# Kernel tuning notes

Hardware: AMD Instinct MI355X
Metric: run time of the kernel (lower is better)

The kernel has to match this reference:

```python
import jax, jax.numpy as jnp
import numpy as np

IGNORE_INDEX = -100
MTP_CE_FACTOR = 0.0
MTP_KL_FACTOR = 1.0

B, S, D, V = 2, 2048, 2048, 32000


def setup_inputs() -> dict:
    key = jax.random.key(0)
    k1, k2, k3, k4 = jax.random.split(key, 4)
    outputs = jax.random.normal(k1, (B, S, D), dtype=jnp.float32)
    mtp_outputs = jax.random.normal(k2, (B, S, D), dtype=jnp.float32)
    # LM-head weight (linear_projection), no bias: logits = h @ W.T
    W = jax.random.normal(k3, (V, D), dtype=jnp.float32) * 0.02
    targets = jax.random.randint(k4, (B, S), 0, V, dtype=jnp.int64)
    return {"outputs": outputs, "mtp_outputs": mtp_outputs, "W": W, "targets": targets}


def reference(outputs, mtp_outputs, W, targets):
    # Flatten tokens: [N, D], [N]
    h = outputs.reshape(-1, outputs.shape[-1])
    mtp_h = mtp_outputs.reshape(-1, mtp_outputs.shape[-1])
    tgt = targets.reshape(-1)

    valid = (tgt != IGNORE_INDEX)                      # [N]
    n_valid = jnp.sum(valid).astype(jnp.float32)
    safe_tgt = jnp.where(valid, tgt, 0)                # in-range gather index

    # Linear projection into vocab logits: [N, V]
    logits = jnp.einsum('nd,vd->nv', h, W)
    mtp_logits = jnp.einsum('nd,vd->nv', mtp_h, W)

    logp = jax.nn.log_softmax(logits, axis=-1)         # [N, V]
    mtp_logp = jax.nn.log_softmax(mtp_logits, axis=-1) # [N, V]

    vmask = valid.astype(jnp.float32)
    # per-token CE (reduction='none', ignore_index masked to 0)
    ce = -jnp.take_along_axis(logp, safe_tgt[:, None], axis=1)[:, 0] * vmask
    mtp_ce = -jnp.take_along_axis(mtp_logp, safe_tgt[:, None], axis=1)[:, 0] * vmask

    # KL(p || q) with p = softmax(logits), q = softmax(mtp_logits), summed over vocab
    p = jnp.exp(logp)
    mtp_kl = jnp.sum(p * (logp - mtp_logp), axis=-1) * vmask

    agreement = (jnp.argmax(logits, axis=-1) == jnp.argmax(mtp_logits, axis=-1)).astype(jnp.float32) * vmask

    # chunked per-chunk sums accumulated == full sum over tokens
    total_loss = (jnp.sum(ce)
                  + MTP_CE_FACTOR * jnp.sum(mtp_ce)
                  + MTP_KL_FACTOR * jnp.sum(mtp_kl)) / n_valid

    ce_mean = jnp.sum(ce) / n_valid
    mtp_ce_mean = jnp.sum(mtp_ce) / n_valid
    mtp_kl_mean = jnp.sum(mtp_kl) / n_valid
    agreement_mean = jnp.sum(agreement) / n_valid
    return (total_loss, ce_mean, mtp_ce_mean, mtp_kl_mean, agreement_mean)
```

## Files before the change

### kernel.cpp

```cpp
#include <hip/hip_runtime.h>
#include <hip/hip_bf16.h>


typedef float f32x4 __attribute__((ext_vector_type(4)));
typedef int v8i __attribute__((ext_vector_type(8)));

#define D_DIM 2048
#define N_TOK 4096
#define V_DIM 32000
#define NVT 250
#define NMT 32

#define W_SCALE 64.0f
#define INV_W_SCALE 0.015625f
#define UNIT_SCALES 0x7F7F7F7F

__device__ __forceinline__ void async_ld16(const void* g, void* l) {
  __builtin_amdgcn_global_load_lds(
      (const __attribute__((address_space(1))) unsigned int*)g,
      (__attribute__((address_space(3))) unsigned int*)l, 16, 0, 0);
}

__global__ void cvt_f32_fp8(const float* __restrict__ s, unsigned char* __restrict__ d,
                            float scale, long n16) {
  long i = (long)blockIdx.x * blockDim.x + threadIdx.x;
  if (i >= n16) return;
  const float4* s4 = (const float4*)s + 4 * i;
  float4 a = s4[0], b = s4[1], c = s4[2], e = s4[3];
  int w0 = __builtin_amdgcn_cvt_pk_fp8_f32(a.x * scale, a.y * scale, 0, 0);
  w0 = __builtin_amdgcn_cvt_pk_fp8_f32(a.z * scale, a.w * scale, w0, 1);
  int w1 = __builtin_amdgcn_cvt_pk_fp8_f32(b.x * scale, b.y * scale, 0, 0);
  w1 = __builtin_amdgcn_cvt_pk_fp8_f32(b.z * scale, b.w * scale, w1, 1);
  int w2 = __builtin_amdgcn_cvt_pk_fp8_f32(c.x * scale, c.y * scale, 0, 0);
  w2 = __builtin_amdgcn_cvt_pk_fp8_f32(c.z * scale, c.w * scale, w2, 1);
  int w3 = __builtin_amdgcn_cvt_pk_fp8_f32(e.x * scale, e.y * scale, 0, 0);
  w3 = __builtin_amdgcn_cvt_pk_fp8_f32(e.z * scale, e.w * scale, w3, 1);
  int4 o; o.x = w0; o.y = w1; o.z = w2; o.w = w3;
  *(int4*)(d + 16 * i) = o;
}

__global__ void tgt_dot(const float* __restrict__ h, const float* __restrict__ mtp,
                        const float* __restrict__ W, const int* __restrict__ tgt,
                        float* __restrict__ tl1, float* __restrict__ tl2) {
  int token = blockIdx.x * 4 + (threadIdx.x >> 6);
  int lane = threadIdx.x & 63;
  int g = tgt[token];
  int sg = g < 0 ? 0 : g;
  const float4* hr = (const float4*)(h + (long)token * D_DIM);
  const float4* mr = (const float4*)(mtp + (long)token * D_DIM);
  const float4* wr = (const float4*)(W + (long)sg * D_DIM);
  float s1 = 0.f, s2 = 0.f;
#pragma unroll
  for (int c = 0; c < 8; ++c) {
    int j = lane + c * 64;
    float4 w = wr[j], a = hr[j], b = mr[j];
    s1 += a.x * w.x + a.y * w.y + a.z * w.z + a.w * w.w;
    s2 += b.x * w.x + b.y * w.y + b.z * w.z + b.w * w.w;
  }
  for (int mask = 1; mask < 64; mask <<= 1) {
    s1 += __shfl_xor(s1, mask, 64);
    s2 += __shfl_xor(s2, mask, 64);
  }
  if (lane == 0) { tl1[token] = s1; tl2[token] = s2; }
}

__global__ __launch_bounds__(256, 2) void fused_gemm(
    const unsigned char* __restrict__ A1, const unsigned char* __restrict__ A2,
    const unsigned char* __restrict__ Bw,
    float* __restrict__ pm1, float* __restrict__ pz1, float* __restrict__ pt,
    float* __restrict__ pi1, float* __restrict__ pm2, float* __restrict__ pz2,
    float* __restrict__ pi2) {
  __shared__ __align__(16) unsigned char sA1[128 * 128];
  __shared__ __align__(16) unsigned char sA2[128 * 128];
  __shared__ __align__(16) unsigned char sB[128 * 128];
  __shared__ float red[128 * 2 * 8];

  const int tid = threadIdx.x;
  const int wave = tid >> 6;
  const int lane = tid & 63;
  const int wm = wave & 1, wn = wave >> 1;
  const int quad = lane >> 4, l15 = lane & 15;

  const int m0 = blockIdx.x * 128;
  const int n0 = blockIdx.y * 128;

  const int srow = wave * 32 + (lane >> 3);
  const int schunk = (lane & 7) ^ ((lane >> 3) & 7);
  const unsigned char* gA1 = A1 + (long)(m0 + srow) * D_DIM + schunk * 16;
  const unsigned char* gA2 = A2 + (long)(m0 + srow) * D_DIM + schunk * 16;
  const unsigned char* gB = Bw + (long)(n0 + srow) * D_DIM + schunk * 16;

  f32x4 acc1[4][4], acc2[4][4];
#pragma unroll
  for (int a = 0; a < 4; ++a)
#pragma unroll
    for (int b = 0; b < 4; ++b) {
      acc1[a][b] = (f32x4){0.f, 0.f, 0.f, 0.f};
      acc2[a][b] = (f32x4){0.f, 0.f, 0.f, 0.f};
    }

  const int sw = l15 & 7;

  for (int ks = 0; ks < D_DIM / 128; ++ks) {
    const int koff = ks * 128;
#pragma unroll
    for (int i = 0; i < 4; ++i) {
      async_ld16(gA1 + (long)i * 8 * D_DIM + koff, &sA1[(wave * 32 + i * 8) * 128]);
      async_ld16(gA2 + (long)i * 8 * D_DIM + koff, &sA2[(wave * 32 + i * 8) * 128]);
      async_ld16(gB + (long)i * 8 * D_DIM + koff, &sB[(wave * 32 + i * 8) * 128]);
    }
    __syncthreads();
    v8i bfr[4];
#pragma unroll
    for (int f = 0; f < 4; ++f) {
      const int rb = (wn * 64 + f * 16 + l15) * 128;
      int4 lo = *(const int4*)&sB[rb + ((quad * 2 + 0) ^ sw) * 16];
      int4 hi = *(const int4*)&sB[rb + ((quad * 2 + 1) ^ sw) * 16];
      bfr[f] = (v8i){lo.x, lo.y, lo.z, lo.w, hi.x, hi.y, hi.z, hi.w};
    }
#pragma unroll
    for (int fm = 0; fm < 4; ++fm) {
      const int ra = (wm * 64 + fm * 16 + l15) * 128;
      int4 lo1 = *(const int4*)&sA1[ra + ((quad * 2 + 0) ^ sw) * 16];
      int4 hi1 = *(const int4*)&sA1[ra + ((quad * 2 + 1) ^ sw) * 16];
      int4 lo2 = *(const int4*)&sA2[ra + ((quad * 2 + 0) ^ sw) * 16];
      int4 hi2 = *(const int4*)&sA2[ra + ((quad * 2 + 1) ^ sw) * 16];
      v8i af1 = (v8i){lo1.x, lo1.y, lo1.z, lo1.w, hi1.x, hi1.y, hi1.z, hi1.w};
      v8i af2 = (v8i){lo2.x, lo2.y, lo2.z, lo2.w, hi2.x, hi2.y, hi2.z, hi2.w};
#pragma unroll
      for (int fn = 0; fn < 4; ++fn) {
        acc1[fm][fn] = __builtin_amdgcn_mfma_scale_f32_16x16x128_f8f6f4(
            af1, bfr[fn], acc1[fm][fn], 0, 0, 0, UNIT_SCALES, 0, UNIT_SCALES);
        acc2[fm][fn] = __builtin_amdgcn_mfma_scale_f32_16x16x128_f8f6f4(
            af2, bfr[fn], acc2[fm][fn], 0, 0, 0, UNIT_SCALES, 0, UNIT_SCALES);
      }
    }
    __syncthreads();
  }

#pragma unroll
  for (int fm = 0; fm < 4; ++fm) {
#pragma unroll
    for (int reg = 0; reg < 4; ++reg) {
      float v1[4], v2[4];
#pragma unroll
      for (int fn = 0; fn < 4; ++fn) {
        v1[fn] = acc1[fm][fn][reg] * INV_W_SCALE;
        v2[fn] = acc2[fm][fn][reg] * INV_W_SCALE;
      }
      float m1 = v1[0]; int b1 = 0;
      float m2 = v2[0]; int b2 = 0;
#pragma unroll
      for (int fn = 1; fn < 4; ++fn) {
        if (v1[fn] > m1) { m1 = v1[fn]; b1 = fn; }
        if (v2[fn] > m2) { m2 = v2[fn]; b2 = fn; }
      }
      float z1 = 0.f, tt = 0.f, z2 = 0.f;
#pragma unroll
      for (int fn = 0; fn < 4; ++fn) {
        float e1 = __expf(v1[fn] - m1);
        z1 += e1;
        tt += e1 * (v1[fn] - v2[fn]);
        z2 += __expf(v2[fn] - m2);
      }
      float i1 = (float)(n0 + wn * 64 + b1 * 16 + l15);
      float i2 = (float)(n0 + wn * 64 + b2 * 16 + l15);
#pragma unroll
      for (int mask = 1; mask <= 8; mask <<= 1) {
        float om1 = __shfl_xor(m1, mask, 64);
        float oz1 = __shfl_xor(z1, mask, 64);
        float ot = __shfl_xor(tt, mask, 64);
        float oi1 = __shfl_xor(i1, mask, 64);
        float om2 = __shfl_xor(m2, mask, 64);
        float oz2 = __shfl_xor(z2, mask, 64);
        float oi2 = __shfl_xor(i2, mask, 64);
        float nm1 = fmaxf(m1, om1);
        float ea = __expf(m1 - nm1), eb = __expf(om1 - nm1);
        z1 = z1 * ea + oz1 * eb;
        tt = tt * ea + ot * eb;
        if (om1 > m1) i1 = oi1;
        m1 = nm1;
        float nm2 = fmaxf(m2, om2);
        float ec = __expf(m2 - nm2), ed = __expf(om2 - nm2);
        z2 = z2 * ec + oz2 * ed;
        if (om2 > m2) i2 = oi2;
        m2 = nm2;
      }
      if (l15 == 0) {
        int row_local = wm * 64 + fm * 16 + quad * 4 + reg;
        float* r = &red[(row_local * 2 + wn) * 8];
        r[0] = m1; r[1] = z1; r[2] = tt; r[3] = i1; r[4] = m2; r[5] = z2; r[6] = i2;
      }
    }
  }
  __syncthreads();
  if (tid < 128) {
    const float* a = &red[(tid * 2 + 0) * 8];
    const float* b = &red[(tid * 2 + 1) * 8];
    float m1 = a[0], z1 = a[1], tt = a[2], i1 = a[3], m2 = a[4], z2 = a[5], i2 = a[6];
    {
      float om1 = b[0], oz1 = b[1], ot = b[2], oi1 = b[3], om2 = b[4], oz2 = b[5], oi2 = b[6];
      float nm1 = fmaxf(m1, om1);
      float ea = __expf(m1 - nm1), eb = __expf(om1 - nm1);
      z1 = z1 * ea + oz1 * eb;
      tt = tt * ea + ot * eb;
      if (om1 > m1) i1 = oi1;
      m1 = nm1;
      float nm2 = fmaxf(m2, om2);
      float ec = __expf(m2 - nm2), ed = __expf(om2 - nm2);
      z2 = z2 * ec + oz2 * ed;
      if (om2 > m2) i2 = oi2;
      m2 = nm2;
    }
    long idx = (long)blockIdx.y * N_TOK + (m0 + tid);
    pm1[idx] = m1; pz1[idx] = z1; pt[idx] = tt; pi1[idx] = i1;
    pm2[idx] = m2; pz2[idx] = z2; pi2[idx] = i2;
  }
}

__global__ void token_combine(const float* __restrict__ pm1, const float* __restrict__ pz1,
                              const float* __restrict__ pt, const float* __restrict__ pi1,
                              const float* __restrict__ pm2, const float* __restrict__ pz2,
                              const float* __restrict__ pi2, const float* __restrict__ tl1,
                              const float* __restrict__ tl2, const int* __restrict__ tgt,
                              float* __restrict__ tout) {
  int t = blockIdx.x * blockDim.x + threadIdx.x;
  if (t >= N_TOK) return;
  float m1 = pm1[t], z1 = pz1[t], tt = pt[t], i1 = pi1[t];
  float m2 = pm2[t], z2 = pz2[t], i2 = pi2[t];
  for (int vt = 1; vt < NVT; ++vt) {
    long o = (long)vt * N_TOK + t;
    float om1 = pm1[o], oz1 = pz1[o], ot = pt[o], oi1 = pi1[o];
    float om2 = pm2[o], oz2 = pz2[o], oi2 = pi2[o];
    float nm1 = fmaxf(m1, om1);
    float ea = __expf(m1 - nm1), eb = __expf(om1 - nm1);
    z1 = z1 * ea + oz1 * eb;
    tt = tt * ea + ot * eb;
    if (om1 > m1) i1 = oi1;
    m1 = nm1;
    float nm2 = fmaxf(m2, om2);
    float ec = __expf(m2 - nm2), ed = __expf(om2 - nm2);
    z2 = z2 * ec + oz2 * ed;
    if (om2 > m2) i2 = oi2;
    m2 = nm2;
  }
  float lse1 = m1 + logf(z1);
  float lse2 = m2 + logf(z2);
  int g = tgt[t];
  float valid = (g != -100) ? 1.f : 0.f;
  float ce = (lse1 - tl1[t]) * valid;
  float mce = (lse2 - tl2[t]) * valid;
  float kl = (lse2 - lse1 + tt / z1) * valid;
  float ag = (i1 == i2) ? valid : 0.f;
  tout[t] = ce;
  tout[N_TOK + t] = mce;
  tout[2 * N_TOK + t] = kl;
  tout[3 * N_TOK + t] = ag;
  tout[4 * N_TOK + t] = valid;
}

__global__ void finalize(const float* __restrict__ tout, float* __restrict__ out) {
  __shared__ float sred[5][4];
  int tid = threadIdx.x;
  float s[5] = {0.f, 0.f, 0.f, 0.f, 0.f};
  for (int i = tid; i < N_TOK; i += 256)
#pragma unroll
    for (int k = 0; k < 5; ++k) s[k] += tout[k * N_TOK + i];
  for (int mask = 1; mask < 64; mask <<= 1)
#pragma unroll
    for (int k = 0; k < 5; ++k) s[k] += __shfl_xor(s[k], mask, 64);
  int wv = tid >> 6, lane = tid & 63;
  if (lane == 0)
#pragma unroll
    for (int k = 0; k < 5; ++k) sred[k][wv] = s[k];
  __syncthreads();
  if (tid == 0) {
    float ce = 0.f, mce = 0.f, kl = 0.f, ag = 0.f, nv = 0.f;
    for (int w = 0; w < 4; ++w) {
      ce += sred[0][w]; mce += sred[1][w]; kl += sred[2][w]; ag += sred[3][w]; nv += sred[4][w];
    }
    out[0] = (ce + 0.0f * mce + 1.0f * kl) / nv;
    out[1] = ce / nv;
    out[2] = mce / nv;
    out[3] = kl / nv;
    out[4] = ag / nv;
  }
}

extern "C" void kernel_launch(void* const* d_in, const int* in_sizes, int n_in,
                              void* d_out, int out_size, void* d_ws, size_t ws_size,
                              hipStream_t stream) {
  const float* h1 = (const float*)d_in[0];
  const float* h2 = (const float*)d_in[1];
  const float* W = (const float*)d_in[2];
  const int* tgt = (const int*)d_in[3];
  float* out = (float*)d_out;
  char* ws = (char*)d_ws;

  const size_t OFF_W = 0;
  const size_t OFF_H1 = 65536000;
  const size_t OFF_H2 = OFF_H1 + 8388608;
  const size_t OFF_P = OFF_H2 + 8388608;
  const size_t PSZ = (size_t)NVT * N_TOK * 4;
  const size_t OFF_TL1 = OFF_P + 7 * PSZ;
  const size_t OFF_TL2 = OFF_TL1 + (size_t)N_TOK * 4;
  const size_t OFF_TOUT = OFF_TL2 + (size_t)N_TOK * 4;

  unsigned char* Wq = (unsigned char*)(ws + OFF_W);
  unsigned char* h1q = (unsigned char*)(ws + OFF_H1);
  unsigned char* h2q = (unsigned char*)(ws + OFF_H2);
  float* pm1 = (float*)(ws + OFF_P + 0 * PSZ);
  float* pz1 = (float*)(ws + OFF_P + 1 * PSZ);
  float* pt = (float*)(ws + OFF_P + 2 * PSZ);
  float* pi1 = (float*)(ws + OFF_P + 3 * PSZ);
  float* pm2 = (float*)(ws + OFF_P + 4 * PSZ);
  float* pz2 = (float*)(ws + OFF_P + 5 * PSZ);
  float* pi2 = (float*)(ws + OFF_P + 6 * PSZ);
  float* tl1 = (float*)(ws + OFF_TL1);
  float* tl2 = (float*)(ws + OFF_TL2);
  float* tout = (float*)(ws + OFF_TOUT);

  {
    long n16w = (long)V_DIM * D_DIM / 16;
    cvt_f32_fp8<<<(n16w + 255) / 256, 256, 0, stream>>>(W, Wq, W_SCALE, n16w);
    long n16h = (long)N_TOK * D_DIM / 16;
    cvt_f32_fp8<<<(n16h + 255) / 256, 256, 0, stream>>>(h1, h1q, 1.0f, n16h);
    cvt_f32_fp8<<<(n16h + 255) / 256, 256, 0, stream>>>(h2, h2q, 1.0f, n16h);
  }
  tgt_dot<<<N_TOK / 4, 256, 0, stream>>>(h1, h2, W, tgt, tl1, tl2);
  {
    dim3 grid(NMT, NVT);
    fused_gemm<<<grid, 256, 0, stream>>>(h1q, h2q, Wq, pm1, pz1, pt, pi1, pm2, pz2, pi2);
  }
  token_combine<<<N_TOK / 256, 256, 0, stream>>>(pm1, pz1, pt, pi1, pm2, pz2, pi2, tl1, tl2, tgt, tout);
  finalize<<<1, 256, 0, stream>>>(tout, out);
}
```

Measured before the change: 1.191 ms.

## Load GEMM tiles in MFMA fragment order and merge fp8 conversion launches

Rewrites the fused GEMM's global-to-LDS staging so each wave copies 16-row by 32-byte fragments laid out in the exact order the MFMA operands are read. Each lane then reads contiguous 16-byte LDS chunks instead of XOR-swizzled rows, which should reduce bank conflicts and address arithmetic. The global loads become less coalesced, since each lane fetches 16 bytes from a different row. It also merges the three fp8 conversion kernels into one launch and pads the reduction scratch stride from 8 to 9 floats.

```diff
diff --git a/kernel.cpp b/kernel.cpp
--- a/kernel.cpp
+++ b/kernel.cpp
@@ -21,10 +21,24 @@
       (__attribute__((address_space(3))) unsigned int*)l, 16, 0, 0);
 }
 
-__global__ void cvt_f32_fp8(const float* __restrict__ s, unsigned char* __restrict__ d,
-                            float scale, long n16) {
+#define NG_W 4096000
+#define NG_H 524288
+__global__ void cvt_all(const float* __restrict__ W, const float* __restrict__ h1,
+                        const float* __restrict__ h2, unsigned char* __restrict__ Wq,
+                        unsigned char* __restrict__ h1q, unsigned char* __restrict__ h2q) {
   long i = (long)blockIdx.x * blockDim.x + threadIdx.x;
-  if (i >= n16) return;
+  const float* s;
+  unsigned char* d;
+  float scale;
+  if (i < NG_W) {
+    s = W; d = Wq; scale = W_SCALE;
+  } else if (i < NG_W + NG_H) {
+    s = h1; d = h1q; scale = 1.0f; i -= NG_W;
+  } else if (i < NG_W + 2 * NG_H) {
+    s = h2; d = h2q; scale = 1.0f; i -= NG_W + NG_H;
+  } else {
+    return;
+  }
   const float4* s4 = (const float4*)s + 4 * i;
   float4 a = s4[0], b = s4[1], c = s4[2], e = s4[3];
   int w0 = __builtin_amdgcn_cvt_pk_fp8_f32(a.x * scale, a.y * scale, 0, 0);
@@ -70,10 +84,10 @@
     float* __restrict__ pm1, float* __restrict__ pz1, float* __restrict__ pt,
     float* __restrict__ pi1, float* __restrict__ pm2, float* __restrict__ pz2,
     float* __restrict__ pi2) {
-  __shared__ __align__(16) unsigned char sA1[128 * 128];
-  __shared__ __align__(16) unsigned char sA2[128 * 128];
-  __shared__ __align__(16) unsigned char sB[128 * 128];
-  __shared__ float red[128 * 2 * 8];
+  __shared__ __align__(16) unsigned char sA1[16384];
+  __shared__ __align__(16) unsigned char sA2[16384];
+  __shared__ __align__(16) unsigned char sB[16384];
+  __shared__ float red[128 * 2 * 9];
 
   const int tid = threadIdx.x;
   const int wave = tid >> 6;
@@ -84,11 +98,27 @@
   const int m0 = blockIdx.x * 128;
   const int n0 = blockIdx.y * 128;
 
-  const int srow = wave * 32 + (lane >> 3);
-  const int schunk = (lane & 7) ^ ((lane >> 3) & 7);
-  const unsigned char* gA1 = A1 + (long)(m0 + srow) * D_DIM + schunk * 16;
-  const unsigned char* gA2 = A2 + (long)(m0 + srow) * D_DIM + schunk * 16;
-  const unsigned char* gB = Bw + (long)(n0 + srow) * D_DIM + schunk * 16;
+  const int voff = (lane & 15) * D_DIM + (lane >> 4) * 32;
+  int rc0, rc1, rc2, rc3;
+  {
+    int r = wave * 4;
+    rc0 = __builtin_amdgcn_readfirstlane(((r >> 3) * 64 + ((r >> 1) & 3) * 16) * D_DIM + (r & 1) * 16);
+    r++;
+    rc1 = __builtin_amdgcn_readfirstlane(((r >> 3) * 64 + ((r >> 1) & 3) * 16) * D_DIM + (r & 1) * 16);
+    r++;
+    rc2 = __builtin_amdgcn_readfirstlane(((r >> 3) * 64 + ((r >> 1) & 3) * 16) * D_DIM + (r & 1) * 16);
+    r++;
+    rc3 = __builtin_amdgcn_readfirstlane(((r >> 3) * 64 + ((r >> 1) & 3) * 16) * D_DIM + (r & 1) * 16);
+  }
+  const unsigned char* gA1 = A1 + (long)m0 * D_DIM + voff;
+  const unsigned char* gA2 = A2 + (long)m0 * D_DIM + voff;
+  const unsigned char* gB = Bw + (long)n0 * D_DIM + voff;
+  unsigned char* dA1 = &sA1[wave * 4096];
+  unsigned char* dA2 = &sA2[wave * 4096];
+  unsigned char* dB = &sB[wave * 4096];
+
+  const int rdA = wm * 8192 + lane * 16;
+  const int rdB = wn * 8192 + lane * 16;
 
   f32x4 acc1[4][4], acc2[4][4];
 #pragma unroll
@@ -99,32 +129,34 @@
       acc2[a][b] = (f32x4){0.f, 0.f, 0.f, 0.f};
     }
 
-  const int sw = l15 & 7;
-
   for (int ks = 0; ks < D_DIM / 128; ++ks) {
     const int koff = ks * 128;
-#pragma unroll
-    for (int i = 0; i < 4; ++i) {
-      async_ld16(gA1 + (long)i * 8 * D_DIM + koff, &sA1[(wave * 32 + i * 8) * 128]);
-      async_ld16(gA2 + (long)i * 8 * D_DIM + koff, &sA2[(wave * 32 + i * 8) * 128]);
-      async_ld16(gB + (long)i * 8 * D_DIM + koff, &sB[(wave * 32 + i * 8) * 128]);
-    }
+    async_ld16(gA1 + rc0 + koff, dA1);
+    async_ld16(gA1 + rc1 + koff, dA1 + 1024);
+    async_ld16(gA1 + rc2 + koff, dA1 + 2048);
+    async_ld16(gA1 + rc3 + koff, dA1 + 3072);
+    async_ld16(gA2 + rc0 + koff, dA2);
+    async_ld16(gA2 + rc1 + koff, dA2 + 1024);
+    async_ld16(gA2 + rc2 + koff, dA2 + 2048);
+    async_ld16(gA2 + rc3 + koff, dA2 + 3072);
+    async_ld16(gB + rc0 + koff, dB);
+    async_ld16(gB + rc1 + koff, dB + 1024);
+    async_ld16(gB + rc2 + koff, dB + 2048);
+    async_ld16(gB + rc3 + koff, dB + 3072);
     __syncthreads();
     v8i bfr[4];
 #pragma unroll
     for (int f = 0; f < 4; ++f) {
-      const int rb = (wn * 64 + f * 16 + l15) * 128;
-      int4 lo = *(const int4*)&sB[rb + ((quad * 2 + 0) ^ sw) * 16];
-      int4 hi = *(const int4*)&sB[rb + ((quad * 2 + 1) ^ sw) * 16];
+      int4 lo = *(const int4*)&sB[rdB + (f * 2 + 0) * 1024];
+      int4 hi = *(const int4*)&sB[rdB + (f * 2 + 1) * 1024];
       bfr[f] = (v8i){lo.x, lo.y, lo.z, lo.w, hi.x, hi.y, hi.z, hi.w};
     }
 #pragma unroll
     for (int fm = 0; fm < 4; ++fm) {
-      const int ra = (wm * 64 + fm * 16 + l15) * 128;
-      int4 lo1 = *(const int4*)&sA1[ra + ((quad * 2 + 0) ^ sw) * 16];
-      int4 hi1 = *(const int4*)&sA1[ra + ((quad * 2 + 1) ^ sw) * 16];
-      int4 lo2 = *(const int4*)&sA2[ra + ((quad * 2 + 0) ^ sw) * 16];
-      int4 hi2 = *(const int4*)&sA2[ra + ((quad * 2 + 1) ^ sw) * 16];
+      int4 lo1 = *(const int4*)&sA1[rdA + (fm * 2 + 0) * 1024];
+      int4 hi1 = *(const int4*)&sA1[rdA + (fm * 2 + 1) * 1024];
+      int4 lo2 = *(const int4*)&sA2[rdA + (fm * 2 + 0) * 1024];
+      int4 hi2 = *(const int4*)&sA2[rdA + (fm * 2 + 1) * 1024];
       v8i af1 = (v8i){lo1.x, lo1.y, lo1.z, lo1.w, hi1.x, hi1.y, hi1.z, hi1.w};
       v8i af2 = (v8i){lo2.x, lo2.y, lo2.z, lo2.w, hi2.x, hi2.y, hi2.z, hi2.w};
 #pragma unroll
@@ -188,15 +220,15 @@
       }
       if (l15 == 0) {
         int row_local = wm * 64 + fm * 16 + quad * 4 + reg;
-        float* r = &red[(row_local * 2 + wn) * 8];
+        float* r = &red[(row_local * 2 + wn) * 9];
         r[0] = m1; r[1] = z1; r[2] = tt; r[3] = i1; r[4] = m2; r[5] = z2; r[6] = i2;
       }
     }
   }
   __syncthreads();
   if (tid < 128) {
-    const float* a = &red[(tid * 2 + 0) * 8];
-    const float* b = &red[(tid * 2 + 1) * 8];
+    const float* a = &red[(tid * 2 + 0) * 9];
+    const float* b = &red[(tid * 2 + 1) * 9];
     float m1 = a[0], z1 = a[1], tt = a[2], i1 = a[3], m2 = a[4], z2 = a[5], i2 = a[6];
     {
       float om1 = b[0], oz1 = b[1], ot = b[2], oi1 = b[3], om2 = b[4], oz2 = b[5], oi2 = b[6];
@@ -321,11 +353,8 @@
   float* tout = (float*)(ws + OFF_TOUT);
 
   {
-    long n16w = (long)V_DIM * D_DIM / 16;
-    cvt_f32_fp8<<<(n16w + 255) / 256, 256, 0, stream>>>(W, Wq, W_SCALE, n16w);
-    long n16h = (long)N_TOK * D_DIM / 16;
-    cvt_f32_fp8<<<(n16h + 255) / 256, 256, 0, stream>>>(h1, h1q, 1.0f, n16h);
-    cvt_f32_fp8<<<(n16h + 255) / 256, 256, 0, stream>>>(h2, h2q, 1.0f, n16h);
+    long ng = NG_W + 2 * NG_H;
+    cvt_all<<<(ng + 255) / 256, 256, 0, stream>>>(W, h1, h2, Wq, h1q, h2q);
   }
   tgt_dot<<<N_TOK / 4, 256, 0, stream>>>(h1, h2, W, tgt, tl1, tl2);
   {
```

Result: slower. 1.334 ms (+12.0%).
